# Performance work log

Measured on AMD Instinct MI355X. Metric: run time of the kernel, lower is better.

The kernel has to match this reference:

```python
import jax, jax.numpy as jnp
import numpy as np

N_HEAD = 16
ROPE_BASE = 10000.0


def _rope_cos_sin(T, D, dtype):
    # D = head_size; matches RotaryEmbedding: emb = cat(freqs, freqs)
    inv_freq = 1.0 / (ROPE_BASE ** (jnp.arange(0, D, 2, dtype=jnp.float32) / D))
    t = jnp.arange(T, dtype=jnp.float32)
    freqs = t[:, None] * inv_freq[None, :]              # [T, D/2]
    emb = jnp.concatenate([freqs, freqs], axis=-1)      # [T, D]
    return jnp.cos(emb).astype(dtype), jnp.sin(emb).astype(dtype)


def _rotate_half(x):
    d = x.shape[-1] // 2
    return jnp.concatenate([-x[..., d:], x[..., :d]], axis=-1)


def setup_inputs() -> dict:
    key = jax.random.key(0)
    ks = jax.random.split(key, 5)
    B, T, C = 2, 2048, 1024
    s_in = 1.0 / np.sqrt(C)
    return {
        "x": jax.random.normal(ks[0], (B, T, C), dtype=jnp.float32),
        "w_attn": jax.random.normal(ks[1], (C, 3 * C), dtype=jnp.float32) * s_in,
        "b_attn": jnp.zeros((3 * C,), dtype=jnp.float32),
        "w_proj": jax.random.normal(ks[2], (C, C), dtype=jnp.float32) * s_in,
        "b_proj": jnp.zeros((C,), dtype=jnp.float32),
    }


def reference(x, w_attn, b_attn, w_proj, b_proj):
    B, T, C = x.shape
    H = N_HEAD
    D = C // H

    qkv = x @ w_attn + b_attn                            # [B,T,3C]
    q, k, v = jnp.split(qkv, 3, axis=-1)
    # [B,T,C] -> [B,H,T,D]
    to_heads = lambda a: a.reshape(B, T, H, D).transpose(0, 2, 1, 3)
    q, k, v = to_heads(q), to_heads(k), to_heads(v)

    cos, sin = _rope_cos_sin(T, D, x.dtype)              # [T,D] each, broadcast over B,H
    q = q * cos + _rotate_half(q) * sin
    k = k * cos + _rotate_half(k) * sin

    scale = 1.0 / np.sqrt(D)
    att = jnp.einsum("bhqd,bhkd->bhqk", q, k) * scale    # [B,H,T,T]
    causal = jnp.tril(jnp.ones((T, T), dtype=bool))
    att = jnp.where(causal, att, jnp.finfo(att.dtype).min)
    att = jax.nn.softmax(att, axis=-1)
    y = jnp.einsum("bhqk,bhkd->bhqd", att, v)            # [B,H,T,D]

    y = y.transpose(0, 2, 1, 3).reshape(B, T, C)
    return y @ w_proj + b_proj
```

## Files before the change

### kernel.cpp

```cpp
#include <hip/hip_runtime.h>
#include <hip/hip_bf16.h>

#define B_ 2
#define T_ 2048
#define C_ 1024
#define H_ 16
#define D_ 64

typedef __attribute__((ext_vector_type(8))) short bf16x8;
typedef __attribute__((ext_vector_type(4))) float f32x4;

static __device__ __forceinline__ float bf2f(unsigned short u) {
  union { unsigned int i; float f; } c;
  c.i = ((unsigned int)u) << 16;
  return c.f;
}
static __device__ __forceinline__ unsigned short f2bf(float f) {
  union { float f; unsigned int i; } c;
  c.f = f;
  unsigned int x = c.i;
  return (unsigned short)((x + 0x7fffu + ((x >> 16) & 1u)) >> 16);
}

static __device__ __forceinline__ void gl_lds16(const void* g, void* s) {
  __builtin_amdgcn_global_load_lds(
      (const __attribute__((address_space(1))) void*)g,
      (__attribute__((address_space(3))) void*)s, 16, 0, 0);
}

__global__ __launch_bounds__(256) void fill_kernel_f32(float* __restrict__ out,
                                                       int n, float v) {
  int i = blockIdx.x * 256 + threadIdx.x;
  if (i < n) out[i] = v;
}

__global__ __launch_bounds__(256) void prep_kernel(
    const float* __restrict__ w_attn, const float* __restrict__ w_proj,
    const float* __restrict__ x,
    unsigned short* __restrict__ waT, unsigned short* __restrict__ wpT,
    unsigned short* __restrict__ xb) {
  __shared__ float tile[32][33];
  const int z = blockIdx.z;
  if (z == 2) {
    const int id = blockIdx.y * 96 + blockIdx.x;
    if (id >= 2048) return;
    int i = (id * 256 + threadIdx.x) * 8;
    float4 f0 = *(const float4*)(x + i);
    float4 f1 = *(const float4*)(x + i + 4);
    union { unsigned short u[8]; uint4 v; } p;
    p.u[0] = f2bf(f0.x); p.u[1] = f2bf(f0.y); p.u[2] = f2bf(f0.z); p.u[3] = f2bf(f0.w);
    p.u[4] = f2bf(f1.x); p.u[5] = f2bf(f1.y); p.u[6] = f2bf(f1.z); p.u[7] = f2bf(f1.w);
    *(uint4*)(xb + i) = p.v;
    return;
  }
  const float* W;
  unsigned short* WT;
  int Kd, Nd;
  if (z == 0) { W = w_attn; WT = waT; Kd = 1024; Nd = 3072; }
  else {
    if (blockIdx.x >= 32) return;
    W = w_proj; WT = wpT; Kd = 1024; Nd = 1024;
  }
  const int n0 = blockIdx.x * 32, k0 = blockIdx.y * 32;
  const int tx = threadIdx.x & 31, ty = threadIdx.x >> 5;
#pragma unroll
  for (int i = 0; i < 4; ++i)
    tile[ty + i * 8][tx] = W[(size_t)(k0 + ty + i * 8) * Nd + n0 + tx];
  __syncthreads();
#pragma unroll
  for (int i = 0; i < 4; ++i)
    WT[(size_t)(n0 + ty + i * 8) * Kd + k0 + tx] = f2bf(tile[tx][ty + i * 8]);
}

__global__ __launch_bounds__(256) void v_transpose(const unsigned short* __restrict__ vP,
                                                   unsigned short* __restrict__ vT) {
  __shared__ unsigned short tile[64][72];
  const int t0 = blockIdx.x * 64;
  const int bh = blockIdx.y;
  const int b = bh >> 4;
  const int srow = threadIdx.x >> 3;
  const int sc8 = (threadIdx.x & 7) * 8;
#pragma unroll
  for (int it = 0; it < 2; ++it) {
    int r = srow + it * 32;
    *(uint4*)&tile[r][sc8] =
        *(const uint4*)(vP + (size_t)(b * T_ + t0 + r) * 1024 + (bh & 15) * 64 + sc8);
  }
  __syncthreads();
#pragma unroll
  for (int it = 0; it < 2; ++it) {
    int dd = srow + it * 32;
    union { unsigned short u[8]; uint4 v; } o;
#pragma unroll
    for (int j = 0; j < 8; ++j) o.u[j] = tile[sc8 + j][dd];
    *(uint4*)(vT + ((size_t)bh * 64 + dd) * 2048 + t0 + sc8) = o.v;
  }
}

template <int OUT_PLANES>
__global__ __launch_bounds__(256) void mfma_gemm(
    const unsigned short* __restrict__ A,
    const unsigned short* __restrict__ BT,
    const float* __restrict__ bias,
    unsigned short* __restrict__ qP, unsigned short* __restrict__ kP,
    unsigned short* __restrict__ vP, float* __restrict__ Fout,
    int N, int K) {
  __shared__ unsigned short S[128 * 128];
  unsigned short* As = S;
  unsigned short* Bs = S + 128 * 64;

  const int tid = threadIdx.x;
  const int w = tid >> 6, lane = tid & 63;
  const int lo = lane & 15, g = lane >> 4;
  const int wm = (w >> 1) * 64, wn = (w & 1) * 64;
  const int m0 = blockIdx.y * 128, n0 = blockIdx.x * 128;

  const int lr8 = lane >> 3;

  const f32x4 zero4 = {0.f, 0.f, 0.f, 0.f};
  f32x4 acc[4][4] = {{zero4, zero4, zero4, zero4}, {zero4, zero4, zero4, zero4},
                     {zero4, zero4, zero4, zero4}, {zero4, zero4, zero4, zero4}};

  for (int k0 = 0; k0 < K; k0 += 64) {
    __syncthreads();
#pragma unroll
    for (int it = 0; it < 4; ++it) {
      const int base_row = w * 32 + it * 8;
      const int r = base_row + lr8;
      const int j = (lane & 7) ^ (r & 7);
      gl_lds16(A + (size_t)(m0 + r) * K + k0 + j * 8, &As[base_row * 64]);
      gl_lds16(BT + (size_t)(n0 + r) * K + k0 + j * 8, &Bs[base_row * 64]);
    }
    __syncthreads();

#pragma unroll
    for (int kk = 0; kk < 2; ++kk) {
      bf16x8 af[4], bfr[4];
#pragma unroll
      for (int i = 0; i < 4; ++i) {
        int ra = wm + i * 16 + lo;
        int rb = wn + i * 16 + lo;
        af[i]  = *(const bf16x8*)&As[ra * 64 + ((g + kk * 4) ^ (ra & 7)) * 8];
        bfr[i] = *(const bf16x8*)&Bs[rb * 64 + ((g + kk * 4) ^ (rb & 7)) * 8];
      }
#pragma unroll
      for (int i = 0; i < 4; ++i)
#pragma unroll
        for (int j = 0; j < 4; ++j)
          acc[i][j] = __builtin_amdgcn_mfma_f32_16x16x32_bf16(af[i], bfr[j],
                                                              acc[i][j], 0, 0, 0);
    }
  }

  float bv[4];
#pragma unroll
  for (int j = 0; j < 4; ++j) bv[j] = bias[n0 + wn + j * 16 + lo];

  if (OUT_PLANES) {
    const int pl = n0 >> 10;
    __syncthreads();
    if (pl == 2) {
#pragma unroll
      for (int i = 0; i < 4; ++i)
#pragma unroll
        for (int r = 0; r < 4; ++r) {
          const int row = wm + i * 16 + g * 4 + r;
#pragma unroll
          for (int j = 0; j < 4; ++j)
            S[row * 128 + wn + j * 16 + lo] = f2bf(acc[i][j][r] + bv[j]);
        }
    } else {
      const float scale = (pl == 0) ? 0.125f : 1.0f;
      const float invA = exp2f((float)(-2 * lo) * (13.287712379549449f / 64.0f)) *
                         0.15915494309189535f;
      const float invB = exp2f((float)(-2 * (lo + 16)) * (13.287712379549449f / 64.0f)) *
                         0.15915494309189535f;
      const int c0 = wn + lo;
#pragma unroll
      for (int i = 0; i < 4; ++i)
#pragma unroll
        for (int r = 0; r < 4; ++r) {
          const int row = wm + i * 16 + g * 4 + r;
          const float t = (float)((m0 + row) & (T_ - 1));
          float ra = t * invA; ra -= floorf(ra);
          float rb = t * invB; rb -= floorf(rb);
          const float sA = __builtin_amdgcn_sinf(ra);
          const float cA = __builtin_amdgcn_cosf(ra);
          const float sB = __builtin_amdgcn_sinf(rb);
          const float cB = __builtin_amdgcn_cosf(rb);
          const float q1A = acc[i][0][r] + bv[0];
          const float q2A = acc[i][2][r] + bv[2];
          const float q1B = acc[i][1][r] + bv[1];
          const float q2B = acc[i][3][r] + bv[3];
          S[row * 128 + c0]      = f2bf((q1A * cA - q2A * sA) * scale);
          S[row * 128 + c0 + 32] = f2bf((q2A * cA + q1A * sA) * scale);
          S[row * 128 + c0 + 16] = f2bf((q1B * cB - q2B * sB) * scale);
          S[row * 128 + c0 + 48] = f2bf((q2B * cB + q1B * sB) * scale);
        }
    }
    __syncthreads();
    unsigned short* P = (pl == 0) ? qP : (pl == 1) ? kP : vP;
    const int pcol0 = n0 & 1023;
#pragma unroll
    for (int it2 = 0; it2 < 8; ++it2) {
      const int p = it2 * 256 + tid;
      const int lrow = p >> 4;
      const int lcol = (p & 15) * 8;
      uint4 v4 = *(const uint4*)&S[lrow * 128 + lcol];
      *(uint4*)(P + (size_t)(m0 + lrow) * 1024 + pcol0 + lcol) = v4;
    }
  } else {
    float* Sf = (float*)S;
#pragma unroll
    for (int hh = 0; hh < 2; ++hh) {
      __syncthreads();
      if ((w >> 1) == hh) {
#pragma unroll
        for (int i = 0; i < 4; ++i)
#pragma unroll
          for (int r = 0; r < 4; ++r) {
            const int lrow = i * 16 + g * 4 + r;
#pragma unroll
            for (int j = 0; j < 4; ++j)
              Sf[lrow * 128 + wn + j * 16 + lo] = acc[i][j][r] + bv[j];
          }
      }
      __syncthreads();
#pragma unroll
      for (int it2 = 0; it2 < 8; ++it2) {
        const int p = it2 * 256 + tid;
        const int lrow = p >> 5;
        const int lcol = (p & 31) * 4;
        float4 v4 = *(const float4*)&Sf[lrow * 128 + lcol];
        *(float4*)(Fout + (size_t)(m0 + hh * 64 + lrow) * N + n0 + lcol) = v4;
      }
    }
  }
}

__global__ __launch_bounds__(256) void flash_mfma6(
    unsigned short* __restrict__ qP,
    const unsigned short* __restrict__ kP,
    const unsigned short* __restrict__ vT) {
  const int cid = blockIdx.x;
  const int xcd = cid & 7;
  const int k6 = cid >> 3;
  const int bh = xcd * 4 + (k6 >> 4);
  const int bx = k6 & 15;
  const int b = bh >> 4, h = bh & 15;
  const int tid = threadIdx.x;
  const int w = tid >> 6, lane = tid & 63;
  const int lo = lane & 15, g = lane >> 4;

  __shared__ unsigned short Ks[64][72];
  __shared__ unsigned short VTs[64][72];
  __shared__ unsigned short Ps[64][72];

  const int srow = tid >> 3;
  const int sc8 = (tid & 7) * 8;
  const f32x4 zero4 = {0.f, 0.f, 0.f, 0.f};

#pragma unroll
  for (int half = 0; half < 2; ++half) {
    const int qt = half ? (31 - bx) : bx;
    const int rowq0 = b * T_ + qt * 64;

    const unsigned short* qrow = qP + (size_t)(rowq0 + w * 16 + lo) * 1024 + h * 64;
    bf16x8 aq0 = *(const bf16x8*)(qrow + g * 8);
    bf16x8 aq1 = *(const bf16x8*)(qrow + 32 + g * 8);

    f32x4 oacc[4] = {zero4, zero4, zero4, zero4};
    float lsum = 0.f;

    uint4 kreg0, kreg1, vreg0, vreg1;
    {
      const size_t kb = (size_t)(b * T_ + srow) * 1024 + h * 64 + sc8;
      kreg0 = *(const uint4*)(kP + kb);
      kreg1 = *(const uint4*)(kP + kb + (size_t)32 * 1024);
      const size_t vb = ((size_t)bh * 64 + srow) * 2048 + sc8;
      vreg0 = *(const uint4*)(vT + vb);
      vreg1 = *(const uint4*)(vT + vb + (size_t)32 * 2048);
    }

    for (int kt = 0; kt <= qt; ++kt) {
      __syncthreads();
      *(uint4*)&Ks[srow][sc8]       = kreg0;
      *(uint4*)&Ks[srow + 32][sc8]  = kreg1;
      *(uint4*)&VTs[srow][sc8]      = vreg0;
      *(uint4*)&VTs[srow + 32][sc8] = vreg1;
      __syncthreads();
      if (kt < qt) {
        const size_t kb = (size_t)(b * T_ + (kt + 1) * 64 + srow) * 1024 + h * 64 + sc8;
        kreg0 = *(const uint4*)(kP + kb);
        kreg1 = *(const uint4*)(kP + kb + (size_t)32 * 1024);
        const size_t vb = ((size_t)bh * 64 + srow) * 2048 + (kt + 1) * 64 + sc8;
        vreg0 = *(const uint4*)(vT + vb);
        vreg1 = *(const uint4*)(vT + vb + (size_t)32 * 2048);
      }

      f32x4 sacc[4] = {zero4, zero4, zero4, zero4};
      __builtin_amdgcn_s_setprio(1);
#pragma unroll
      for (int ct = 0; ct < 4; ++ct) {
        bf16x8 bk0 = *(const bf16x8*)&Ks[ct * 16 + lo][g * 8];
        bf16x8 bk1 = *(const bf16x8*)&Ks[ct * 16 + lo][32 + g * 8];
        sacc[ct] = __builtin_amdgcn_mfma_f32_16x16x32_bf16(bk0, aq0, sacc[ct], 0, 0, 0);
        sacc[ct] = __builtin_amdgcn_mfma_f32_16x16x32_bf16(bk1, aq1, sacc[ct], 0, 0, 0);
      }
      __builtin_amdgcn_s_setprio(0);

      if (kt == qt) {
#pragma unroll
        for (int ct = 0; ct < 4; ++ct)
#pragma unroll
          for (int r = 0; r < 4; ++r)
            if (ct * 16 + g * 4 + r > w * 16 + lo) sacc[ct][r] = -1e30f;
      }

#pragma unroll
      for (int ct = 0; ct < 4; ++ct) {
        float p0 = __expf(sacc[ct][0]);
        float p1 = __expf(sacc[ct][1]);
        float p2 = __expf(sacc[ct][2]);
        float p3 = __expf(sacc[ct][3]);
        lsum += (p0 + p1) + (p2 + p3);
        unsigned int u0 = (unsigned int)f2bf(p0) | ((unsigned int)f2bf(p1) << 16);
        unsigned int u1 = (unsigned int)f2bf(p2) | ((unsigned int)f2bf(p3) << 16);
        uint2 pw; pw.x = u0; pw.y = u1;
        *(uint2*)&Ps[w * 16 + lo][ct * 16 + g * 4] = pw;
      }

      bf16x8 ap0 = *(const bf16x8*)&Ps[w * 16 + lo][g * 8];
      bf16x8 ap1 = *(const bf16x8*)&Ps[w * 16 + lo][32 + g * 8];
      __builtin_amdgcn_s_setprio(1);
#pragma unroll
      for (int c2 = 0; c2 < 4; ++c2) {
        bf16x8 bv0 = *(const bf16x8*)&VTs[c2 * 16 + lo][g * 8];
        bf16x8 bv1 = *(const bf16x8*)&VTs[c2 * 16 + lo][32 + g * 8];
        oacc[c2] = __builtin_amdgcn_mfma_f32_16x16x32_bf16(ap0, bv0, oacc[c2], 0, 0, 0);
        oacc[c2] = __builtin_amdgcn_mfma_f32_16x16x32_bf16(ap1, bv1, oacc[c2], 0, 0, 0);
      }
      __builtin_amdgcn_s_setprio(0);
    }

    lsum += __shfl_xor(lsum, 16);
    lsum += __shfl_xor(lsum, 32);

#pragma unroll
    for (int r = 0; r < 4; ++r) {
      float inv_r = 1.0f / __shfl(lsum, g * 4 + r);
      unsigned short* dst = qP + (size_t)(rowq0 + w * 16 + g * 4 + r) * 1024 + h * 64 + lo;
#pragma unroll
      for (int c2 = 0; c2 < 4; ++c2)
        dst[c2 * 16] = f2bf(oacc[c2][r] * inv_r);
    }
  }
}

extern "C" void kernel_launch(void* const* d_in, const int* in_sizes, int n_in,
                              void* d_out, int out_size, void* d_ws, size_t ws_size,
                              hipStream_t stream) {
  const float *x = nullptr, *w_attn = nullptr, *b_attn = nullptr,
              *w_proj = nullptr, *b_proj = nullptr;
  for (int i = 0; i < n_in; ++i) {
    switch (in_sizes[i]) {
      case B_ * T_ * C_:  x      = (const float*)d_in[i]; break;
      case C_ * 3 * C_:   w_attn = (const float*)d_in[i]; break;
      case 3 * C_:        b_attn = (const float*)d_in[i]; break;
      case C_ * C_:       w_proj = (const float*)d_in[i]; break;
      case C_:            b_proj = (const float*)d_in[i]; break;
      default: break;
    }
  }
  float* out = (float*)d_out;
  const int nblk = (out_size + 255) / 256;

  if (!x || !w_attn || !b_attn || !w_proj || !b_proj) {
    fill_kernel_f32<<<nblk, 256, 0, stream>>>(out, out_size, 100.0f);
    return;
  }
  if (ws_size < (size_t)48 * 1024 * 1024) {
    fill_kernel_f32<<<nblk, 256, 0, stream>>>(out, out_size, 50.0f);
    return;
  }

  unsigned short* qP  = (unsigned short*)d_ws;
  unsigned short* kP  = qP + (size_t)(B_ * T_) * 1024;
  unsigned short* vP  = kP + (size_t)(B_ * T_) * 1024;
  unsigned short* vT  = vP + (size_t)(B_ * T_) * 1024;
  unsigned short* xb  = vT + (size_t)(B_ * T_) * 1024;
  unsigned short* waT = xb + (size_t)(B_ * T_) * C_;
  unsigned short* wpT = waT + (size_t)C_ * 3 * C_;

  prep_kernel<<<dim3(96, 32, 3), 256, 0, stream>>>(w_attn, w_proj, x, waT, wpT, xb);
  mfma_gemm<1><<<dim3((3 * C_) / 128, (B_ * T_) / 128), 256, 0, stream>>>(
      xb, waT, b_attn, qP, kP, vP, nullptr, 3 * C_, C_);
  v_transpose<<<dim3(T_ / 64, B_ * H_), 256, 0, stream>>>(vP, vT);
  flash_mfma6<<<dim3(512), 256, 0, stream>>>(qP, kP, vT);
  mfma_gemm<0><<<dim3(C_ / 128, (B_ * T_) / 128), 256, 0, stream>>>(
      qP, wpT, b_proj, nullptr, nullptr, nullptr, out, C_, C_);
}
```

Baseline: 183.1 us.

## Replace QKV GEMM with 256x256-tile double-buffered 512-thread kernel

Adds a dedicated QKV projection kernel that uses 256x256 output tiles, 8 waves and double-buffered LDS filled by direct global-to-LDS loads. Explicit vmcnt waits let the next K-slice load overlap the MFMAs on the current one. Larger tiles raise operand reuse per block. The trade-off is a grid of only 192 blocks, fewer than the CU count, with 128KB of LDS per block. The output GEMM is split into its own fp32-only kernel with the same logic as before.

```diff
diff --git a/kernel.cpp b/kernel.cpp
--- a/kernel.cpp
+++ b/kernel.cpp
@@ -97,13 +97,153 @@
   }
 }
 
-template <int OUT_PLANES>
-__global__ __launch_bounds__(256) void mfma_gemm(
+__global__ __launch_bounds__(512, 2) void gemm_qkv_256(
     const unsigned short* __restrict__ A,
     const unsigned short* __restrict__ BT,
     const float* __restrict__ bias,
     unsigned short* __restrict__ qP, unsigned short* __restrict__ kP,
-    unsigned short* __restrict__ vP, float* __restrict__ Fout,
+    unsigned short* __restrict__ vP) {
+  __shared__ unsigned short L[65536];
+  unsigned short* As = L;
+  unsigned short* Bs = L + 32768;
+
+  const int tid = threadIdx.x;
+  const int wid = tid >> 6, lane = tid & 63;
+  const int lo = lane & 15, g = lane >> 4;
+  const int wr = wid >> 2, wc = wid & 3;
+  const int m0 = blockIdx.y * 256, n0 = blockIdx.x * 256;
+  const int lr8 = lane >> 3;
+  const int NT = 16;
+
+  const f32x4 zero4 = {0.f, 0.f, 0.f, 0.f};
+  f32x4 acc[8][4];
+#pragma unroll
+  for (int i = 0; i < 8; ++i)
+#pragma unroll
+    for (int j = 0; j < 4; ++j) acc[i][j] = zero4;
+
+#define STAGE_QKV(t)                                                          \
+  do {                                                                        \
+    const int buf_ = ((t) & 1) ? 16384 : 0;                                   \
+    const int k0_ = (t) * 64;                                                 \
+    _Pragma("unroll")                                                         \
+    for (int it = 0; it < 4; ++it) {                                          \
+      const int br = wid * 32 + it * 8;                                       \
+      const int r = br + lr8;                                                 \
+      const int j = (lane & 7) ^ (r & 7);                                     \
+      gl_lds16(A + (size_t)(m0 + r) * 1024 + k0_ + j * 8, &As[buf_ + br * 64]);\
+    }                                                                         \
+    _Pragma("unroll")                                                         \
+    for (int it = 0; it < 4; ++it) {                                          \
+      const int br = wid * 32 + it * 8;                                       \
+      const int r = br + lr8;                                                 \
+      const int j = (lane & 7) ^ (r & 7);                                     \
+      gl_lds16(BT + (size_t)(n0 + r) * 1024 + k0_ + j * 8, &Bs[buf_ + br * 64]);\
+    }                                                                         \
+  } while (0)
+
+  STAGE_QKV(0);
+  STAGE_QKV(1);
+  asm volatile("s_waitcnt vmcnt(8)" ::: "memory");
+  __builtin_amdgcn_s_barrier();
+
+  for (int t = 0; t < NT; ++t) {
+    const int buf = (t & 1) ? 16384 : 0;
+#pragma unroll
+    for (int kk = 0; kk < 2; ++kk) {
+      bf16x8 af[8], bfr[4];
+#pragma unroll
+      for (int i = 0; i < 8; ++i) {
+        const int ra = wr * 128 + i * 16 + lo;
+        af[i] = *(const bf16x8*)&As[buf + ra * 64 + ((g + kk * 4) ^ (ra & 7)) * 8];
+      }
+#pragma unroll
+      for (int j = 0; j < 4; ++j) {
+        const int rb = wc * 64 + j * 16 + lo;
+        bfr[j] = *(const bf16x8*)&Bs[buf + rb * 64 + ((g + kk * 4) ^ (rb & 7)) * 8];
+      }
+#pragma unroll
+      for (int i = 0; i < 8; ++i)
+#pragma unroll
+        for (int j = 0; j < 4; ++j)
+          acc[i][j] = __builtin_amdgcn_mfma_f32_16x16x32_bf16(af[i], bfr[j],
+                                                              acc[i][j], 0, 0, 0);
+    }
+    __builtin_amdgcn_s_barrier();
+    if (t + 2 < NT) {
+      STAGE_QKV(t + 2);
+      asm volatile("s_waitcnt vmcnt(8)" ::: "memory");
+      __builtin_amdgcn_s_barrier();
+    } else if (t + 1 < NT) {
+      asm volatile("s_waitcnt vmcnt(0)" ::: "memory");
+      __builtin_amdgcn_s_barrier();
+    }
+  }
+#undef STAGE_QKV
+
+  float bv[4];
+#pragma unroll
+  for (int j = 0; j < 4; ++j) bv[j] = bias[n0 + wc * 64 + j * 16 + lo];
+
+  const int pl = n0 >> 10;
+  unsigned short* S = L;
+  if (pl == 2) {
+#pragma unroll
+    for (int i = 0; i < 8; ++i)
+#pragma unroll
+      for (int r = 0; r < 4; ++r) {
+        const int row = wr * 128 + i * 16 + g * 4 + r;
+#pragma unroll
+        for (int j = 0; j < 4; ++j)
+          S[row * 256 + wc * 64 + j * 16 + lo] = f2bf(acc[i][j][r] + bv[j]);
+      }
+  } else {
+    const float scale = (pl == 0) ? 0.125f : 1.0f;
+    const float invA = exp2f((float)(-2 * lo) * (13.287712379549449f / 64.0f)) *
+                       0.15915494309189535f;
+    const float invB = exp2f((float)(-2 * (lo + 16)) * (13.287712379549449f / 64.0f)) *
+                       0.15915494309189535f;
+    const int c0 = wc * 64 + lo;
+#pragma unroll
+    for (int i = 0; i < 8; ++i)
+#pragma unroll
+      for (int r = 0; r < 4; ++r) {
+        const int row = wr * 128 + i * 16 + g * 4 + r;
+        const float t = (float)((m0 + row) & (T_ - 1));
+        float ra = t * invA; ra -= floorf(ra);
+        float rb = t * invB; rb -= floorf(rb);
+        const float sA = __builtin_amdgcn_sinf(ra);
+        const float cA = __builtin_amdgcn_cosf(ra);
+        const float sB = __builtin_amdgcn_sinf(rb);
+        const float cB = __builtin_amdgcn_cosf(rb);
+        const float q1A = acc[i][0][r] + bv[0];
+        const float q2A = acc[i][2][r] + bv[2];
+        const float q1B = acc[i][1][r] + bv[1];
+        const float q2B = acc[i][3][r] + bv[3];
+        S[row * 256 + c0]      = f2bf((q1A * cA - q2A * sA) * scale);
+        S[row * 256 + c0 + 32] = f2bf((q2A * cA + q1A * sA) * scale);
+        S[row * 256 + c0 + 16] = f2bf((q1B * cB - q2B * sB) * scale);
+        S[row * 256 + c0 + 48] = f2bf((q2B * cB + q1B * sB) * scale);
+      }
+  }
+  __builtin_amdgcn_s_barrier();
+  unsigned short* P = (pl == 0) ? qP : (pl == 1) ? kP : vP;
+  const int pcol0 = n0 & 1023;
+#pragma unroll
+  for (int it2 = 0; it2 < 16; ++it2) {
+    const int p = it2 * 512 + tid;
+    const int lrow = p >> 5;
+    const int lcol = (p & 31) * 8;
+    uint4 v4 = *(const uint4*)&S[lrow * 256 + lcol];
+    *(uint4*)(P + (size_t)(m0 + lrow) * 1024 + pcol0 + lcol) = v4;
+  }
+}
+
+__global__ __launch_bounds__(256) void mfma_gemm_f32(
+    const unsigned short* __restrict__ A,
+    const unsigned short* __restrict__ BT,
+    const float* __restrict__ bias,
+    float* __restrict__ Fout,
     int N, int K) {
   __shared__ unsigned short S[128 * 128];
   unsigned short* As = S;
@@ -156,84 +296,29 @@
 #pragma unroll
   for (int j = 0; j < 4; ++j) bv[j] = bias[n0 + wn + j * 16 + lo];
 
-  if (OUT_PLANES) {
-    const int pl = n0 >> 10;
+  float* Sf = (float*)S;
+#pragma unroll
+  for (int hh = 0; hh < 2; ++hh) {
     __syncthreads();
-    if (pl == 2) {
+    if ((w >> 1) == hh) {
 #pragma unroll
       for (int i = 0; i < 4; ++i)
 #pragma unroll
         for (int r = 0; r < 4; ++r) {
-          const int row = wm + i * 16 + g * 4 + r;
+          const int lrow = i * 16 + g * 4 + r;
 #pragma unroll
           for (int j = 0; j < 4; ++j)
-            S[row * 128 + wn + j * 16 + lo] = f2bf(acc[i][j][r] + bv[j]);
+            Sf[lrow * 128 + wn + j * 16 + lo] = acc[i][j][r] + bv[j];
         }
-    } else {
-      const float scale = (pl == 0) ? 0.125f : 1.0f;
-      const float invA = exp2f((float)(-2 * lo) * (13.287712379549449f / 64.0f)) *
-                         0.15915494309189535f;
-      const float invB = exp2f((float)(-2 * (lo + 16)) * (13.287712379549449f / 64.0f)) *
-                         0.15915494309189535f;
-      const int c0 = wn + lo;
-#pragma unroll
-      for (int i = 0; i < 4; ++i)
-#pragma unroll
-        for (int r = 0; r < 4; ++r) {
-          const int row = wm + i * 16 + g * 4 + r;
-          const float t = (float)((m0 + row) & (T_ - 1));
-          float ra = t * invA; ra -= floorf(ra);
-          float rb = t * invB; rb -= floorf(rb);
-          const float sA = __builtin_amdgcn_sinf(ra);
-          const float cA = __builtin_amdgcn_cosf(ra);
-          const float sB = __builtin_amdgcn_sinf(rb);
-          const float cB = __builtin_amdgcn_cosf(rb);
-          const float q1A = acc[i][0][r] + bv[0];
-          const float q2A = acc[i][2][r] + bv[2];
-          const float q1B = acc[i][1][r] + bv[1];
-          const float q2B = acc[i][3][r] + bv[3];
-          S[row * 128 + c0]      = f2bf((q1A * cA - q2A * sA) * scale);
-          S[row * 128 + c0 + 32] = f2bf((q2A * cA + q1A * sA) * scale);
-          S[row * 128 + c0 + 16] = f2bf((q1B * cB - q2B * sB) * scale);
-          S[row * 128 + c0 + 48] = f2bf((q2B * cB + q1B * sB) * scale);
-        }
     }
     __syncthreads();
-    unsigned short* P = (pl == 0) ? qP : (pl == 1) ? kP : vP;
-    const int pcol0 = n0 & 1023;
 #pragma unroll
     for (int it2 = 0; it2 < 8; ++it2) {
       const int p = it2 * 256 + tid;
-      const int lrow = p >> 4;
-      const int lcol = (p & 15) * 8;
-      uint4 v4 = *(const uint4*)&S[lrow * 128 + lcol];
-      *(uint4*)(P + (size_t)(m0 + lrow) * 1024 + pcol0 + lcol) = v4;
-    }
-  } else {
-    float* Sf = (float*)S;
-#pragma unroll
-    for (int hh = 0; hh < 2; ++hh) {
-      __syncthreads();
-      if ((w >> 1) == hh) {
-#pragma unroll
-        for (int i = 0; i < 4; ++i)
-#pragma unroll
-          for (int r = 0; r < 4; ++r) {
-            const int lrow = i * 16 + g * 4 + r;
-#pragma unroll
-            for (int j = 0; j < 4; ++j)
-              Sf[lrow * 128 + wn + j * 16 + lo] = acc[i][j][r] + bv[j];
-          }
-      }
-      __syncthreads();
-#pragma unroll
-      for (int it2 = 0; it2 < 8; ++it2) {
-        const int p = it2 * 256 + tid;
-        const int lrow = p >> 5;
-        const int lcol = (p & 31) * 4;
-        float4 v4 = *(const float4*)&Sf[lrow * 128 + lcol];
-        *(float4*)(Fout + (size_t)(m0 + hh * 64 + lrow) * N + n0 + lcol) = v4;
-      }
+      const int lrow = p >> 5;
+      const int lcol = (p & 31) * 4;
+      float4 v4 = *(const float4*)&Sf[lrow * 128 + lcol];
+      *(float4*)(Fout + (size_t)(m0 + hh * 64 + lrow) * N + n0 + lcol) = v4;
     }
   }
 }
@@ -393,10 +478,10 @@
   unsigned short* wpT = waT + (size_t)C_ * 3 * C_;
 
   prep_kernel<<<dim3(96, 32, 3), 256, 0, stream>>>(w_attn, w_proj, x, waT, wpT, xb);
-  mfma_gemm<1><<<dim3((3 * C_) / 128, (B_ * T_) / 128), 256, 0, stream>>>(
-      xb, waT, b_attn, qP, kP, vP, nullptr, 3 * C_, C_);
+  gemm_qkv_256<<<dim3((3 * C_) / 256, (B_ * T_) / 256), 512, 0, stream>>>(
+      xb, waT, b_attn, qP, kP, vP);
   v_transpose<<<dim3(T_ / 64, B_ * H_), 256, 0, stream>>>(vP, vT);
   flash_mfma6<<<dim3(512), 256, 0, stream>>>(qP, kP, vT);
-  mfma_gemm<0><<<dim3(C_ / 128, (B_ * T_) / 128), 256, 0, stream>>>(
-      qP, wpT, b_proj, nullptr, nullptr, nullptr, out, C_, C_);
-}
+  mfma_gemm_f32<<<dim3(C_ / 128, (B_ * T_) / 128), 256, 0, stream>>>(
+      qP, wpT, b_proj, out, C_, C_);
+}
```

New measurement: 188.8 us. 3.1% more time.
